# Kernel optimization log

Hardware: AMD Instinct MI355X
Metric: run time of the kernel (lower is better)

Reference implementation:

```python
import jax, jax.numpy as jnp
import numpy as np

D = 1024
H = 16
HD = D // H
EPS = 1e-5

def _layernorm(x, g, b):
    xf = x.astype(jnp.float32)
    mu = jnp.mean(xf, axis=-1, keepdims=True)
    var = jnp.mean(jnp.square(xf - mu), axis=-1, keepdims=True)
    return ((xf - mu) * jax.lax.rsqrt(var + EPS) * g + b).astype(x.dtype)

def setup_inputs() -> dict:
    key = jax.random.key(0)
    ks = jax.random.split(key, 12)
    B, S = 4, 1024
    s_in = 1.0 / np.sqrt(D)
    inp = {
        "x": jax.random.normal(ks[0], (B, S, D), dtype=jnp.float32),
        "in_proj_w": jax.random.normal(ks[1], (3 * D, D), dtype=jnp.float32) * s_in,
        "in_proj_b": jnp.zeros((3 * D,), dtype=jnp.float32),
        "out_w": jax.random.normal(ks[2], (D, D), dtype=jnp.float32) * s_in,
        "out_b": jnp.zeros((D,), dtype=jnp.float32),
        "ln1_g": jnp.ones((D,), dtype=jnp.float32),
        "ln1_b": jnp.zeros((D,), dtype=jnp.float32),
        "fc_w": jax.random.normal(ks[3], (4 * D, D), dtype=jnp.float32) * s_in,
        "fc_b": jnp.zeros((4 * D,), dtype=jnp.float32),
        "proj_w": jax.random.normal(ks[4], (D, 4 * D), dtype=jnp.float32) * (1.0 / np.sqrt(4 * D)),
        "proj_b": jnp.zeros((D,), dtype=jnp.float32),
        "ln2_g": jnp.ones((D,), dtype=jnp.float32),
        "ln2_b": jnp.zeros((D,), dtype=jnp.float32),
    }
    return inp

def reference(x, in_proj_w, in_proj_b, out_w, out_b, ln1_g, ln1_b,
              fc_w, fc_b, proj_w, proj_b, ln2_g, ln2_b):
    B, S, _ = x.shape
    scaling = float(HD) ** -0.5
    # --- attention sublayer ---
    h = _layernorm(x, ln1_g, ln1_b)
    qkv = h @ in_proj_w.T + in_proj_b              # [B,S,3D]
    q, k, v = jnp.split(qkv, 3, axis=-1)
    q = (q * scaling).reshape(B, S, H, HD).transpose(0, 2, 1, 3)  # [B,H,S,hd]
    k = k.reshape(B, S, H, HD).transpose(0, 2, 1, 3)
    v = v.reshape(B, S, H, HD).transpose(0, 2, 1, 3)
    attn = jax.nn.softmax(jnp.einsum('bhqd,bhkd->bhqk', q, k), axis=-1)
    o = jnp.einsum('bhqk,bhkd->bhqd', attn, v).transpose(0, 2, 1, 3).reshape(B, S, D)
    x = x + o @ out_w.T + out_b
    # --- MLP sublayer (QuickGELU) ---
    h = _layernorm(x, ln2_g, ln2_b)
    u = h @ fc_w.T + fc_b                          # [B,S,4D]
    u = u * jax.nn.sigmoid(1.702 * u)
    x = x + u @ proj_w.T + proj_b
    return x
```

## Files before the change

### kernel.cpp

```cpp
#include <hip/hip_runtime.h>
#include <math.h>

#define D_MODEL 1024
#define SEQ     1024
#define BATCH   4
#define NTOK    (BATCH * SEQ)

typedef __bf16 bf16;
using bfrag = __attribute__((ext_vector_type(8))) __bf16;
using ffrag = __attribute__((ext_vector_type(4))) float;

__device__ __forceinline__ ffrag mfma16(bfrag a, bfrag b, ffrag c) {
  return __builtin_amdgcn_mfma_f32_16x16x32_bf16(a, b, c, 0, 0, 0);
}

__device__ __forceinline__ void gload_lds16(const void* g, void* l) {
  __builtin_amdgcn_global_load_lds(
      (const __attribute__((address_space(1))) void*)g,
      (__attribute__((address_space(3))) void*)l, 16, 0, 0);
}

__global__ void convert_all(const float* __restrict__ s0, bf16* __restrict__ d0, int n0,
                            const float* __restrict__ s1, bf16* __restrict__ d1, int n1,
                            const float* __restrict__ s2, bf16* __restrict__ d2, int n2,
                            const float* __restrict__ s3, bf16* __restrict__ d3, int n3,
                            float scale, int limit0) {
  const float* src; bf16* dst; int n; int limit = 0;
  switch (blockIdx.y) {
    case 0: src = s0; dst = d0; n = n0; limit = limit0; break;
    case 1: src = s1; dst = d1; n = n1; break;
    case 2: src = s2; dst = d2; n = n2; break;
    default: src = s3; dst = d3; n = n3; break;
  }
  int i = blockIdx.x * blockDim.x + threadIdx.x;
  const int stride = gridDim.x * blockDim.x;
  for (; i < n; i += stride) {
    float4 v = ((const float4*)src)[i];
    float sc = (i < limit) ? scale : 1.0f;
    bf16* d = dst + (size_t)i * 4;
    d[0] = (bf16)(v.x * sc); d[1] = (bf16)(v.y * sc);
    d[2] = (bf16)(v.z * sc); d[3] = (bf16)(v.w * sc);
  }
}

__global__ void scale_bias(const float* __restrict__ src, float* __restrict__ dst,
                           int n, int limit, float scale) {
  int i = blockIdx.x * blockDim.x + threadIdx.x;
  if (i < n) dst[i] = src[i] * (i < limit ? scale : 1.0f);
}

__global__ __launch_bounds__(256) void ln_row(const float* __restrict__ x,
                                              const float* __restrict__ gamma,
                                              const float* __restrict__ beta,
                                              bf16* __restrict__ out) {
  const int row = blockIdx.x, tid = threadIdx.x;
  const float4 v = ((const float4*)(x + (size_t)row * D_MODEL))[tid];
  float s  = v.x + v.y + v.z + v.w;
  float ss = v.x * v.x + v.y * v.y + v.z * v.z + v.w * v.w;
#pragma unroll
  for (int off = 32; off >= 1; off >>= 1) {
    s  += __shfl_xor(s, off);
    ss += __shfl_xor(ss, off);
  }
  __shared__ float rs[4], rss[4];
  const int w = tid >> 6;
  if ((tid & 63) == 0) { rs[w] = s; rss[w] = ss; }
  __syncthreads();
  s  = rs[0] + rs[1] + rs[2] + rs[3];
  ss = rss[0] + rss[1] + rss[2] + rss[3];
  const float mu   = s * (1.0f / D_MODEL);
  const float var  = ss * (1.0f / D_MODEL) - mu * mu;
  const float rstd = rsqrtf(var + 1e-5f);
  const float4 gv = ((const float4*)gamma)[tid];
  const float4 bv = ((const float4*)beta)[tid];
  bf16* o = out + (size_t)row * D_MODEL + tid * 4;
  o[0] = (bf16)((v.x - mu) * rstd * gv.x + bv.x);
  o[1] = (bf16)((v.y - mu) * rstd * gv.y + bv.y);
  o[2] = (bf16)((v.z - mu) * rstd * gv.z + bv.z);
  o[3] = (bf16)((v.w - mu) * rstd * gv.w + bv.w);
}

template <int EPI>
__global__ __launch_bounds__(256, 2) void gemm_bt(
    const bf16* __restrict__ A, const bf16* __restrict__ B,
    const float* __restrict__ bias, const float* __restrict__ resid,
    float* __restrict__ outF, bf16* __restrict__ outB,
    int M, int N, int K) {
  __shared__ bf16 As[2][128 * 32];
  __shared__ bf16 Bs[2][128 * 32];
  const int tid = threadIdx.x;
  const int lane = tid & 63, w = tid >> 6;
  const int wm = w >> 1, wn = w & 1;
  const int ql = lane & 15, lg = lane >> 4;
  const int m0 = blockIdx.x * 128, n0 = blockIdx.y * 128;

  ffrag acc[4][4];
#pragma unroll
  for (int i = 0; i < 4; i++)
#pragma unroll
    for (int j = 0; j < 4; j++) acc[i][j] = ffrag{0.f, 0.f, 0.f, 0.f};

  const int r0 = tid >> 2;
  const int jsw = (tid & 3) ^ (r0 & 3);
  const bf16* a0 = A + (size_t)(m0 + r0) * K + jsw * 8;
  const bf16* a1 = A + (size_t)(m0 + 64 + r0) * K + jsw * 8;
  const bf16* b0 = B + (size_t)(n0 + r0) * K + jsw * 8;
  const bf16* b1 = B + (size_t)(n0 + 64 + r0) * K + jsw * 8;
  const int lo = w * 512;

  auto STAGE = [&](int bs, int kk) {
    gload_lds16(a0 + kk, &As[bs][lo]);
    gload_lds16(a1 + kk, &As[bs][2048 + lo]);
    gload_lds16(b0 + kk, &Bs[bs][lo]);
    gload_lds16(b1 + kk, &Bs[bs][2048 + lo]);
  };

  STAGE(0, 0);
  __syncthreads();

  int cur = 0;
  for (int k0 = 0; k0 < K; k0 += 32) {
    if (k0 + 32 < K) STAGE(cur ^ 1, k0 + 32);
    bfrag af[4], bfr[4];
#pragma unroll
    for (int i = 0; i < 4; i++) {
      const int row = wm * 64 + i * 16 + ql;
      af[i] = *(const bfrag*)&As[cur][row * 32 + ((lg ^ (row & 3)) * 8)];
    }
#pragma unroll
    for (int j = 0; j < 4; j++) {
      const int row = wn * 64 + j * 16 + ql;
      bfr[j] = *(const bfrag*)&Bs[cur][row * 32 + ((lg ^ (row & 3)) * 8)];
    }
#pragma unroll
    for (int i = 0; i < 4; i++)
#pragma unroll
      for (int j = 0; j < 4; j++)
        acc[i][j] = mfma16(af[i], bfr[j], acc[i][j]);
    __syncthreads();
    cur ^= 1;
  }

#pragma unroll
  for (int i = 0; i < 4; i++) {
    const int row = m0 + wm * 64 + i * 16 + lg * 4;
#pragma unroll
    for (int j = 0; j < 4; j++) {
      const int col = n0 + wn * 64 + j * 16 + ql;
      const float bv = bias[col];
#pragma unroll
      for (int r = 0; r < 4; r++) {
        float v = acc[i][j][r] + bv;
        const size_t idx = (size_t)(row + r) * N + col;
        if (EPI == 0) {
          outB[idx] = (bf16)v;
        } else if (EPI == 1) {
          outF[idx] = v + resid[idx];
        } else {
          outB[idx] = (bf16)(v / (1.0f + __expf(-1.702f * v)));
        }
      }
    }
  }
}

template <int EPI>
__global__ __launch_bounds__(256, 4) void gemm_bt64(
    const bf16* __restrict__ A, const bf16* __restrict__ B,
    const float* __restrict__ bias, const float* __restrict__ resid,
    float* __restrict__ outF, bf16* __restrict__ outB,
    int M, int N, int K) {
  __shared__ bf16 As[2][64 * 64];
  __shared__ bf16 Bs[2][64 * 64];
  const int tid = threadIdx.x;
  const int lane = tid & 63, w = tid >> 6;
  const int wm = w >> 1, wn = w & 1;
  const int ql = lane & 15, lg = lane >> 4;
  const int m0 = blockIdx.x * 64, n0 = blockIdx.y * 64;

  ffrag acc[2][2];
#pragma unroll
  for (int i = 0; i < 2; i++)
#pragma unroll
    for (int j = 0; j < 2; j++) acc[i][j] = ffrag{0.f, 0.f, 0.f, 0.f};

  const int r0 = tid >> 3;
  const int jsw = ((tid & 7) ^ (r0 & 7)) * 8;
  const bf16* a0 = A + (size_t)(m0 + r0) * K + jsw;
  const bf16* a1 = A + (size_t)(m0 + 32 + r0) * K + jsw;
  const bf16* b0 = B + (size_t)(n0 + r0) * K + jsw;
  const bf16* b1 = B + (size_t)(n0 + 32 + r0) * K + jsw;
  const int lo = tid * 8;

  auto STAGE = [&](int bs, int kk) {
    gload_lds16(a0 + kk, &As[bs][lo]);
    gload_lds16(a1 + kk, &As[bs][2048 + lo]);
    gload_lds16(b0 + kk, &Bs[bs][lo]);
    gload_lds16(b1 + kk, &Bs[bs][2048 + lo]);
  };

  STAGE(0, 0);
  __syncthreads();

  int cur = 0;
  for (int k0 = 0; k0 < K; k0 += 64) {
    if (k0 + 64 < K) STAGE(cur ^ 1, k0 + 64);
    bfrag af[2][2], bfr[2][2];
#pragma unroll
    for (int i = 0; i < 2; i++) {
      const int row = wm * 32 + i * 16 + ql;
      const int r7 = row & 7;
#pragma unroll
      for (int kc = 0; kc < 2; kc++)
        af[i][kc] = *(const bfrag*)&As[cur][row * 64 + (((lg + 4 * kc) ^ r7) * 8)];
    }
#pragma unroll
    for (int j = 0; j < 2; j++) {
      const int row = wn * 32 + j * 16 + ql;
      const int r7 = row & 7;
#pragma unroll
      for (int kc = 0; kc < 2; kc++)
        bfr[j][kc] = *(const bfrag*)&Bs[cur][row * 64 + (((lg + 4 * kc) ^ r7) * 8)];
    }
#pragma unroll
    for (int kc = 0; kc < 2; kc++)
#pragma unroll
      for (int i = 0; i < 2; i++)
#pragma unroll
        for (int j = 0; j < 2; j++)
          acc[i][j] = mfma16(af[i][kc], bfr[j][kc], acc[i][j]);
    __syncthreads();
    cur ^= 1;
  }

#pragma unroll
  for (int i = 0; i < 2; i++) {
    const int row = m0 + wm * 32 + i * 16 + lg * 4;
#pragma unroll
    for (int j = 0; j < 2; j++) {
      const int col = n0 + wn * 32 + j * 16 + ql;
      const float bv = bias[col];
#pragma unroll
      for (int r = 0; r < 4; r++) {
        float v = acc[i][j][r] + bv;
        const size_t idx = (size_t)(row + r) * N + col;
        if (EPI == 0) {
          outB[idx] = (bf16)v;
        } else if (EPI == 1) {
          outF[idx] = v + resid[idx];
        } else {
          outB[idx] = (bf16)(v / (1.0f + __expf(-1.702f * v)));
        }
      }
    }
  }
}

__global__ __launch_bounds__(256) void transpose_v(const bf16* __restrict__ qkv,
                                                   bf16* __restrict__ vt) {
  __shared__ bf16 T[64 * 66];
  const int tid = threadIdx.x;
  const int bh = blockIdx.y, b = bh >> 4, h = bh & 15;
  const int s0 = blockIdx.x * 64;
  const bf16* src = qkv + (size_t)b * SEQ * 3072 + 2048 + h * 64;

  const int sl = tid >> 3, c = tid & 7;
#pragma unroll
  for (int p = 0; p < 2; p++) {
    const int s = sl + p * 32;
    const bfrag v = *(const bfrag*)(src + (size_t)(s0 + s) * 3072 + c * 8);
#pragma unroll
    for (int e = 0; e < 8; e++) T[s * 66 + c * 8 + e] = v[e];
  }
  __syncthreads();
  bf16* dst = vt + (size_t)bh * 64 * 1024;
#pragma unroll
  for (int p = 0; p < 2; p++) {
    const int d = sl + p * 32;
    bfrag o;
#pragma unroll
    for (int e = 0; e < 8; e++) o[e] = T[(c * 8 + e) * 66 + d];
    *(bfrag*)(dst + (size_t)d * 1024 + s0 + c * 8) = o;
  }
}

__global__ __launch_bounds__(256, 3) void flash_attn(const bf16* __restrict__ qkv,
                                                     const bf16* __restrict__ vt,
                                                     bf16* __restrict__ o) {
  __shared__ bf16 Kl[128 * 64];
  __shared__ bf16 Vl[64 * 128];
  __shared__ bf16 Pl[4 * 16 * 136];
  const int tid = threadIdx.x, lane = tid & 63, wid = tid >> 6;
  const int ql = lane & 15, lg = lane >> 4;
  const int bh = blockIdx.y, b = bh >> 4, h = bh & 15;
  const int qrow0 = blockIdx.x * 64 + wid * 16;
  const size_t headq = (size_t)b * SEQ * 3072 + (size_t)h * 64;

  const bf16* qp = qkv + headq + (size_t)(qrow0 + ql) * 3072 + lg * 8;
  const bfrag q0 = *(const bfrag*)qp;
  const bfrag q1 = *(const bfrag*)(qp + 32);

  float mrun[4], lrun[4];
  ffrag oacc[4];
#pragma unroll
  for (int r = 0; r < 4; r++) { mrun[r] = -1e30f; lrun[r] = 0.0f; }
#pragma unroll
  for (int f = 0; f < 4; f++) oacc[f] = ffrag{0.f, 0.f, 0.f, 0.f};

  const int kr0 = tid >> 3;
  const int kjsw = ((tid & 7) ^ (kr0 & 7)) * 8;
  const bf16* kp = qkv + headq + 1024 + (size_t)kr0 * 3072 + kjsw;
  const int vr_ = tid >> 4, vlc = tid & 15;
  const bf16* vhead = vt + (size_t)bh * 64 * 1024;
  bf16* Pw = Pl + wid * 2176;

  for (int kt = 0; kt < SEQ; kt += 128) {
#pragma unroll
    for (int pp = 0; pp < 4; pp++)
      gload_lds16(kp + (size_t)(kt + pp * 32) * 3072, &Kl[pp * 2048 + tid * 8]);
#pragma unroll
    for (int pp = 0; pp < 4; pp++) {
      const int vr = pp * 16 + vr_;
      const int gc = vlc ^ (vr & 7);
      gload_lds16(vhead + (size_t)vr * 1024 + kt + gc * 8, &Vl[(pp * 256 + tid) * 8]);
    }
    __syncthreads();

    ffrag sa[8];
    __builtin_amdgcn_s_setprio(1);
#pragma unroll
    for (int sub = 0; sub < 8; sub++) {
      const int krow = sub * 16 + ql;
      const int r7 = krow & 7;
      const bfrag kf0 = *(const bfrag*)&Kl[krow * 64 + ((lg ^ r7) * 8)];
      const bfrag kf1 = *(const bfrag*)&Kl[krow * 64 + (((lg + 4) ^ r7) * 8)];
      ffrag s4 = ffrag{0.f, 0.f, 0.f, 0.f};
      s4 = mfma16(q0, kf0, s4);
      s4 = mfma16(q1, kf1, s4);
      sa[sub] = s4;
    }
    __builtin_amdgcn_s_setprio(0);

    float lmax[4];
#pragma unroll
    for (int r = 0; r < 4; r++) {
      float m = sa[0][r];
#pragma unroll
      for (int sub = 1; sub < 8; sub++) m = fmaxf(m, sa[sub][r]);
      lmax[r] = m;
    }
    bool ok = (lmax[0] - mrun[0] <= 8.0f) && (lmax[1] - mrun[1] <= 8.0f) &&
              (lmax[2] - mrun[2] <= 8.0f) && (lmax[3] - mrun[3] <= 8.0f);
    if (!__all(ok)) {
#pragma unroll
      for (int r = 0; r < 4; r++) {
        float mx = lmax[r];
        mx = fmaxf(mx, __shfl_xor(mx, 1));
        mx = fmaxf(mx, __shfl_xor(mx, 2));
        mx = fmaxf(mx, __shfl_xor(mx, 4));
        mx = fmaxf(mx, __shfl_xor(mx, 8));
        const float mnew = fmaxf(mrun[r], mx);
        const float corr = exp2f(mrun[r] - mnew);
        lrun[r] *= corr;
#pragma unroll
        for (int f = 0; f < 4; f++) oacc[f][r] *= corr;
        mrun[r] = mnew;
      }
    }
#pragma unroll
    for (int r = 0; r < 4; r++) {
      float pv[8], srow = 0.f;
#pragma unroll
      for (int sub = 0; sub < 8; sub++) {
        pv[sub] = exp2f(sa[sub][r] - mrun[r]);
        srow += pv[sub];
      }
      srow += __shfl_xor(srow, 1);
      srow += __shfl_xor(srow, 2);
      srow += __shfl_xor(srow, 4);
      srow += __shfl_xor(srow, 8);
      lrun[r] += srow;
      bf16* prow = Pw + (lg * 4 + r) * 136;
#pragma unroll
      for (int sub = 0; sub < 8; sub++) prow[sub * 16 + ql] = (bf16)pv[sub];
    }

    bfrag pa[4];
#pragma unroll
    for (int kc = 0; kc < 4; kc++)
      pa[kc] = *(const bfrag*)&Pw[ql * 136 + kc * 32 + lg * 8];
    __builtin_amdgcn_s_setprio(1);
#pragma unroll
    for (int f = 0; f < 4; f++) {
      const int vrow = f * 16 + ql;
      const int r7 = vrow & 7;
#pragma unroll
      for (int kc = 0; kc < 4; kc++) {
        const bfrag vf = *(const bfrag*)&Vl[vrow * 128 + (((kc * 4 + lg) ^ r7) * 8)];
        oacc[f] = mfma16(pa[kc], vf, oacc[f]);
      }
    }
    __builtin_amdgcn_s_setprio(0);
    __syncthreads();
  }

#pragma unroll
  for (int f = 0; f < 4; f++) {
#pragma unroll
    for (int r = 0; r < 4; r++) {
      const size_t orow = (size_t)b * SEQ + qrow0 + lg * 4 + r;
      o[orow * 1024 + h * 64 + f * 16 + ql] = (bf16)(oacc[f][r] / lrun[r]);
    }
  }
}

extern "C" void kernel_launch(void* const* d_in, const int* in_sizes, int n_in,
                              void* d_out, int out_size, void* d_ws, size_t ws_size,
                              hipStream_t stream) {
  (void)in_sizes; (void)n_in; (void)out_size; (void)ws_size;
  const float* x      = (const float*)d_in[0];
  const float* in_w   = (const float*)d_in[1];
  const float* in_b   = (const float*)d_in[2];
  const float* out_w  = (const float*)d_in[3];
  const float* out_b  = (const float*)d_in[4];
  const float* ln1_g  = (const float*)d_in[5];
  const float* ln1_b  = (const float*)d_in[6];
  const float* fc_w   = (const float*)d_in[7];
  const float* fc_b   = (const float*)d_in[8];
  const float* proj_w = (const float*)d_in[9];
  const float* proj_b = (const float*)d_in[10];
  const float* ln2_g  = (const float*)d_in[11];
  const float* ln2_b  = (const float*)d_in[12];
  float* out = (float*)d_out;

  char* p = (char*)d_ws;
  auto alloc = [&](size_t bytes) { char* r = p; p += (bytes + 255) & ~255ull; return r; };
  bf16* w_qkv  = (bf16*)alloc((size_t)3072 * 1024 * 2);
  bf16* w_out  = (bf16*)alloc((size_t)1024 * 1024 * 2);
  bf16* w_fc   = (bf16*)alloc((size_t)4096 * 1024 * 2);
  bf16* w_proj = (bf16*)alloc((size_t)1024 * 4096 * 2);
  float* b_qkv = (float*)alloc((size_t)3072 * 4);
  bf16* hbuf   = (bf16*)alloc((size_t)NTOK * 1024 * 2);
  float* x2    = (float*)alloc((size_t)NTOK * 1024 * 4);
  bf16* qkv    = (bf16*)alloc((size_t)NTOK * 3072 * 2);
  bf16* aout   = (bf16*)alloc((size_t)NTOK * 1024 * 2);
  bf16* ubuf   = qkv;
  bf16* vtb    = (bf16*)x2;

  const float scaling = 0.125f * 1.44269504089f;
  convert_all<<<dim3(1024, 4), 256, 0, stream>>>(
      in_w, w_qkv, 3072 * 1024 / 4,
      out_w, w_out, 1024 * 1024 / 4,
      fc_w, w_fc, 4096 * 1024 / 4,
      proj_w, w_proj, 4096 * 1024 / 4,
      scaling, 1024 * 1024 / 4);
  scale_bias<<<12, 256, 0, stream>>>(in_b, b_qkv, 3072, 1024, scaling);

  ln_row<<<NTOK, 256, 0, stream>>>(x, ln1_g, ln1_b, hbuf);
  gemm_bt<0><<<dim3(32, 24), 256, 0, stream>>>(hbuf, w_qkv, b_qkv, nullptr,
                                               nullptr, qkv, NTOK, 3072, 1024);
  transpose_v<<<dim3(16, 64), 256, 0, stream>>>(qkv, vtb);
  flash_attn<<<dim3(16, 64), 256, 0, stream>>>(qkv, vtb, aout);
  gemm_bt64<1><<<dim3(64, 16), 256, 0, stream>>>(aout, w_out, out_b, x,
                                                 x2, nullptr, NTOK, 1024, 1024);
  ln_row<<<NTOK, 256, 0, stream>>>(x2, ln2_g, ln2_b, hbuf);
  gemm_bt<2><<<dim3(32, 32), 256, 0, stream>>>(hbuf, w_fc, fc_b, nullptr,
                                               nullptr, ubuf, NTOK, 4096, 1024);
  gemm_bt64<1><<<dim3(64, 16), 256, 0, stream>>>(ubuf, w_proj, proj_b, x2,
                                                 out, nullptr, NTOK, 1024, 4096);
}
```

Baseline: 233.9 us.

## Split-K the MLP down-projection with 128x128 tiles and defer softmax row-sum reduction

The final proj GEMM (K=4096) now uses the 128x128 tile kernel with a two-way split over K, writing fp32 partials to workspace. A separate reduce kernel then adds the partials, bias and residual. This trades the 64x64 tile kernel for larger tiles with better data reuse, at the cost of extra partial-buffer traffic and one more launch, and it only runs if the workspace is large enough. In flash attention, the per-iteration cross-lane shuffle reduction of row sums is moved to a single reduction after the loop, and the final division becomes a multiply by the reciprocal.

```diff
diff --git a/kernel.cpp b/kernel.cpp
--- a/kernel.cpp
+++ b/kernel.cpp
@@ -93,6 +93,8 @@
   const int wm = w >> 1, wn = w & 1;
   const int ql = lane & 15, lg = lane >> 4;
   const int m0 = blockIdx.x * 128, n0 = blockIdx.y * 128;
+  const int Klen = (EPI == 3) ? (K >> 1) : K;
+  const int kz0  = (EPI == 3) ? blockIdx.z * Klen : 0;
 
   ffrag acc[4][4];
 #pragma unroll
@@ -102,10 +104,10 @@
 
   const int r0 = tid >> 2;
   const int jsw = (tid & 3) ^ (r0 & 3);
-  const bf16* a0 = A + (size_t)(m0 + r0) * K + jsw * 8;
-  const bf16* a1 = A + (size_t)(m0 + 64 + r0) * K + jsw * 8;
-  const bf16* b0 = B + (size_t)(n0 + r0) * K + jsw * 8;
-  const bf16* b1 = B + (size_t)(n0 + 64 + r0) * K + jsw * 8;
+  const bf16* a0 = A + (size_t)(m0 + r0) * K + kz0 + jsw * 8;
+  const bf16* a1 = A + (size_t)(m0 + 64 + r0) * K + kz0 + jsw * 8;
+  const bf16* b0 = B + (size_t)(n0 + r0) * K + kz0 + jsw * 8;
+  const bf16* b1 = B + (size_t)(n0 + 64 + r0) * K + kz0 + jsw * 8;
   const int lo = w * 512;
 
   auto STAGE = [&](int bs, int kk) {
@@ -119,8 +121,8 @@
   __syncthreads();
 
   int cur = 0;
-  for (int k0 = 0; k0 < K; k0 += 32) {
-    if (k0 + 32 < K) STAGE(cur ^ 1, k0 + 32);
+  for (int k0 = 0; k0 < Klen; k0 += 32) {
+    if (k0 + 32 < Klen) STAGE(cur ^ 1, k0 + 32);
     bfrag af[4], bfr[4];
 #pragma unroll
     for (int i = 0; i < 4; i++) {
@@ -141,13 +143,14 @@
     cur ^= 1;
   }
 
+  const size_t zoff = (EPI == 3) ? (size_t)blockIdx.z * M * N : 0;
 #pragma unroll
   for (int i = 0; i < 4; i++) {
     const int row = m0 + wm * 64 + i * 16 + lg * 4;
 #pragma unroll
     for (int j = 0; j < 4; j++) {
       const int col = n0 + wn * 64 + j * 16 + ql;
-      const float bv = bias[col];
+      const float bv = (EPI == 3) ? 0.0f : bias[col];
 #pragma unroll
       for (int r = 0; r < 4; r++) {
         float v = acc[i][j][r] + bv;
@@ -156,11 +159,35 @@
           outB[idx] = (bf16)v;
         } else if (EPI == 1) {
           outF[idx] = v + resid[idx];
+        } else if (EPI == 3) {
+          outF[zoff + idx] = v;
         } else {
           outB[idx] = (bf16)(v / (1.0f + __expf(-1.702f * v)));
         }
       }
     }
+  }
+}
+
+__global__ __launch_bounds__(256) void splitk_reduce(const float* __restrict__ part,
+                                                     const float* __restrict__ bias,
+                                                     const float* __restrict__ resid,
+                                                     float* __restrict__ out,
+                                                     int mn4, int n4mask) {
+  int i = blockIdx.x * 256 + threadIdx.x;
+  const int stride = gridDim.x * 256;
+  const float4* p0 = (const float4*)part;
+  const float4* p1 = p0 + mn4;
+  const float4* rv = (const float4*)resid;
+  const float4* bv = (const float4*)bias;
+  for (; i < mn4; i += stride) {
+    const float4 a = p0[i], b = p1[i], r = rv[i], c = bv[i & n4mask];
+    float4 o;
+    o.x = a.x + b.x + r.x + c.x;
+    o.y = a.y + b.y + r.y + c.y;
+    o.z = a.z + b.z + r.z + c.z;
+    o.w = a.w + b.w + r.w + c.w;
+    ((float4*)out)[i] = o;
   }
 }
 
@@ -369,20 +396,15 @@
     }
 #pragma unroll
     for (int r = 0; r < 4; r++) {
-      float pv[8], srow = 0.f;
+      float srow = 0.f;
+      bf16* prow = Pw + (lg * 4 + r) * 136;
 #pragma unroll
       for (int sub = 0; sub < 8; sub++) {
-        pv[sub] = exp2f(sa[sub][r] - mrun[r]);
-        srow += pv[sub];
+        const float pv = exp2f(sa[sub][r] - mrun[r]);
+        srow += pv;
+        prow[sub * 16 + ql] = (bf16)pv;
       }
-      srow += __shfl_xor(srow, 1);
-      srow += __shfl_xor(srow, 2);
-      srow += __shfl_xor(srow, 4);
-      srow += __shfl_xor(srow, 8);
       lrun[r] += srow;
-      bf16* prow = Pw + (lg * 4 + r) * 136;
-#pragma unroll
-      for (int sub = 0; sub < 8; sub++) prow[sub * 16 + ql] = (bf16)pv[sub];
     }
 
     bfrag pa[4];
@@ -404,12 +426,22 @@
     __syncthreads();
   }
 
+  float rinv[4];
+#pragma unroll
+  for (int r = 0; r < 4; r++) {
+    float ls = lrun[r];
+    ls += __shfl_xor(ls, 1);
+    ls += __shfl_xor(ls, 2);
+    ls += __shfl_xor(ls, 4);
+    ls += __shfl_xor(ls, 8);
+    rinv[r] = 1.0f / ls;
+  }
 #pragma unroll
   for (int f = 0; f < 4; f++) {
 #pragma unroll
     for (int r = 0; r < 4; r++) {
       const size_t orow = (size_t)b * SEQ + qrow0 + lg * 4 + r;
-      o[orow * 1024 + h * 64 + f * 16 + ql] = (bf16)(oacc[f][r] / lrun[r]);
+      o[orow * 1024 + h * 64 + f * 16 + ql] = (bf16)(oacc[f][r] * rinv[r]);
     }
   }
 }
@@ -417,7 +449,7 @@
 extern "C" void kernel_launch(void* const* d_in, const int* in_sizes, int n_in,
                               void* d_out, int out_size, void* d_ws, size_t ws_size,
                               hipStream_t stream) {
-  (void)in_sizes; (void)n_in; (void)out_size; (void)ws_size;
+  (void)in_sizes; (void)n_in; (void)out_size;
   const float* x      = (const float*)d_in[0];
   const float* in_w   = (const float*)d_in[1];
   const float* in_b   = (const float*)d_in[2];
@@ -446,6 +478,8 @@
   bf16* aout   = (bf16*)alloc((size_t)NTOK * 1024 * 2);
   bf16* ubuf   = qkv;
   bf16* vtb    = (bf16*)x2;
+  float* partials = (float*)alloc((size_t)2 * NTOK * 1024 * 4);
+  const bool use_splitk = (size_t)(p - (char*)d_ws) <= ws_size;
 
   const float scaling = 0.125f * 1.44269504089f;
   convert_all<<<dim3(1024, 4), 256, 0, stream>>>(
@@ -466,6 +500,13 @@
   ln_row<<<NTOK, 256, 0, stream>>>(x2, ln2_g, ln2_b, hbuf);
   gemm_bt<2><<<dim3(32, 32), 256, 0, stream>>>(hbuf, w_fc, fc_b, nullptr,
                                                nullptr, ubuf, NTOK, 4096, 1024);
-  gemm_bt64<1><<<dim3(64, 16), 256, 0, stream>>>(ubuf, w_proj, proj_b, x2,
-                                                 out, nullptr, NTOK, 1024, 4096);
-}
+  if (use_splitk) {
+    gemm_bt<3><<<dim3(32, 8, 2), 256, 0, stream>>>(ubuf, w_proj, nullptr, nullptr,
+                                                   partials, nullptr, NTOK, 1024, 4096);
+    splitk_reduce<<<2048, 256, 0, stream>>>(partials, proj_b, x2, out,
+                                            NTOK * 1024 / 4, 255);
+  } else {
+    gemm_bt64<1><<<dim3(64, 16), 256, 0, stream>>>(ubuf, w_proj, proj_b, x2,
+                                                   out, nullptr, NTOK, 1024, 4096);
+  }
+}
```

Result: slower. 242.9 us (+3.8%).

## Remap workgroups across XCDs, fix LDS swizzle, defer softmax row-sum reduction

Applied to the files above, without the earlier changes.

Remaps the flat workgroup index so that consecutive tiles land on the same XCD in both GEMM kernels and in flash attention, aiming for better L2 reuse of shared A/B panels and K/V heads. Changes the 128-tile GEMM LDS swizzle to XOR with (row>>1)&3, meant to reduce bank conflicts for 64-byte rows. In flash attention, the per-iteration cross-lane row-sum shuffles are moved to a single reduction after the loop, and the final divide becomes a multiply by a reciprocal. The XCD remap assumes the workgroup count is divisible by 8.

```diff
diff --git a/kernel.cpp b/kernel.cpp
--- a/kernel.cpp
+++ b/kernel.cpp
@@ -18,6 +18,10 @@
   __builtin_amdgcn_global_load_lds(
       (const __attribute__((address_space(1))) void*)g,
       (__attribute__((address_space(3))) void*)l, 16, 0, 0);
+}
+
+__device__ __forceinline__ int xcd_remap(int flat, int nwg) {
+  return (flat & 7) * (nwg >> 3) + (flat >> 3);
 }
 
 __global__ void convert_all(const float* __restrict__ s0, bf16* __restrict__ d0, int n0,
@@ -92,7 +96,9 @@
   const int lane = tid & 63, w = tid >> 6;
   const int wm = w >> 1, wn = w & 1;
   const int ql = lane & 15, lg = lane >> 4;
-  const int m0 = blockIdx.x * 128, n0 = blockIdx.y * 128;
+  const int nwg = gridDim.x * gridDim.y;
+  const int flat = xcd_remap(blockIdx.y * gridDim.x + blockIdx.x, nwg);
+  const int m0 = (flat % gridDim.x) * 128, n0 = (flat / gridDim.x) * 128;
 
   ffrag acc[4][4];
 #pragma unroll
@@ -101,7 +107,7 @@
     for (int j = 0; j < 4; j++) acc[i][j] = ffrag{0.f, 0.f, 0.f, 0.f};
 
   const int r0 = tid >> 2;
-  const int jsw = (tid & 3) ^ (r0 & 3);
+  const int jsw = (tid & 3) ^ ((r0 >> 1) & 3);
   const bf16* a0 = A + (size_t)(m0 + r0) * K + jsw * 8;
   const bf16* a1 = A + (size_t)(m0 + 64 + r0) * K + jsw * 8;
   const bf16* b0 = B + (size_t)(n0 + r0) * K + jsw * 8;
@@ -125,12 +131,12 @@
 #pragma unroll
     for (int i = 0; i < 4; i++) {
       const int row = wm * 64 + i * 16 + ql;
-      af[i] = *(const bfrag*)&As[cur][row * 32 + ((lg ^ (row & 3)) * 8)];
+      af[i] = *(const bfrag*)&As[cur][row * 32 + ((lg ^ ((row >> 1) & 3)) * 8)];
     }
 #pragma unroll
     for (int j = 0; j < 4; j++) {
       const int row = wn * 64 + j * 16 + ql;
-      bfr[j] = *(const bfrag*)&Bs[cur][row * 32 + ((lg ^ (row & 3)) * 8)];
+      bfr[j] = *(const bfrag*)&Bs[cur][row * 32 + ((lg ^ ((row >> 1) & 3)) * 8)];
     }
 #pragma unroll
     for (int i = 0; i < 4; i++)
@@ -176,7 +182,9 @@
   const int lane = tid & 63, w = tid >> 6;
   const int wm = w >> 1, wn = w & 1;
   const int ql = lane & 15, lg = lane >> 4;
-  const int m0 = blockIdx.x * 64, n0 = blockIdx.y * 64;
+  const int nwg = gridDim.x * gridDim.y;
+  const int flat = xcd_remap(blockIdx.y * gridDim.x + blockIdx.x, nwg);
+  const int m0 = (flat % gridDim.x) * 64, n0 = (flat / gridDim.x) * 64;
 
   ffrag acc[2][2];
 #pragma unroll
@@ -292,8 +300,9 @@
   __shared__ bf16 Pl[4 * 16 * 136];
   const int tid = threadIdx.x, lane = tid & 63, wid = tid >> 6;
   const int ql = lane & 15, lg = lane >> 4;
-  const int bh = blockIdx.y, b = bh >> 4, h = bh & 15;
-  const int qrow0 = blockIdx.x * 64 + wid * 16;
+  const int flat = xcd_remap(blockIdx.y * 16 + blockIdx.x, 1024);
+  const int bh = flat >> 4, b = bh >> 4, h = bh & 15;
+  const int qrow0 = (flat & 15) * 64 + wid * 16;
   const size_t headq = (size_t)b * SEQ * 3072 + (size_t)h * 64;
 
   const bf16* qp = qkv + headq + (size_t)(qrow0 + ql) * 3072 + lg * 8;
@@ -369,20 +378,15 @@
     }
 #pragma unroll
     for (int r = 0; r < 4; r++) {
-      float pv[8], srow = 0.f;
+      float srow = 0.f;
+      bf16* prow = Pw + (lg * 4 + r) * 136;
 #pragma unroll
       for (int sub = 0; sub < 8; sub++) {
-        pv[sub] = exp2f(sa[sub][r] - mrun[r]);
-        srow += pv[sub];
+        const float pv = exp2f(sa[sub][r] - mrun[r]);
+        srow += pv;
+        prow[sub * 16 + ql] = (bf16)pv;
       }
-      srow += __shfl_xor(srow, 1);
-      srow += __shfl_xor(srow, 2);
-      srow += __shfl_xor(srow, 4);
-      srow += __shfl_xor(srow, 8);
       lrun[r] += srow;
-      bf16* prow = Pw + (lg * 4 + r) * 136;
-#pragma unroll
-      for (int sub = 0; sub < 8; sub++) prow[sub * 16 + ql] = (bf16)pv[sub];
     }
 
     bfrag pa[4];
@@ -404,12 +408,22 @@
     __syncthreads();
   }
 
+  float rinv[4];
+#pragma unroll
+  for (int r = 0; r < 4; r++) {
+    float ls = lrun[r];
+    ls += __shfl_xor(ls, 1);
+    ls += __shfl_xor(ls, 2);
+    ls += __shfl_xor(ls, 4);
+    ls += __shfl_xor(ls, 8);
+    rinv[r] = 1.0f / ls;
+  }
 #pragma unroll
   for (int f = 0; f < 4; f++) {
 #pragma unroll
     for (int r = 0; r < 4; r++) {
       const size_t orow = (size_t)b * SEQ + qrow0 + lg * 4 + r;
-      o[orow * 1024 + h * 64 + f * 16 + ql] = (bf16)(oacc[f][r] / lrun[r]);
+      o[orow * 1024 + h * 64 + f * 16 + ql] = (bf16)(oacc[f][r] * rinv[r]);
     }
   }
 }
```

Measured after the change: 231.5 us. About the same (-1.0%).
